# Optimization experiments

Hardware: AMD Instinct MI355X
Metric: run time of the kernel (lower is better)

## Reference

```python
import jax, jax.numpy as jnp
import numpy as np

TOPK_RATIOS = (0.67, 0.75, 0.8)


def setup_inputs() -> dict:
    key = jax.random.key(0)
    k0, k1, k2 = jax.random.split(key, 3)
    B, L, S, H, E, D = 4, 2048, 2048, 8, 64, 64
    queries = jax.random.normal(k0, (B, L, H, E), dtype=jnp.float32)
    keys = jax.random.normal(k1, (B, S, H, E), dtype=jnp.float32)
    values = jax.random.normal(k2, (B, S, H, D), dtype=jnp.float32)
    attn_weights = jnp.ones((len(TOPK_RATIOS),), dtype=jnp.float32)  # nn.Parameter(ones)
    attn_mask = jnp.zeros((1,), dtype=bool)  # unused by the module
    return {"queries": queries, "keys": keys, "values": values,
            "attn_weights": attn_weights, "attn_mask": attn_mask}


def reference(queries, keys, values, attn_weights, attn_mask):
    # queries: [B,L,H,E], keys: [B,S,H,E], values: [B,S,H,D]
    B, L, H, E = queries.shape
    S = keys.shape[1]
    scale = 1.0 / np.sqrt(E)  # self.scale is None -> 1/sqrt(E)
    scores = jnp.einsum('blhe,bshe->bhls', queries, keys) * scale  # [B,H,L,S]
    out = jnp.zeros(queries.shape[:3] + (values.shape[-1],), dtype=scores.dtype)
    for i, ratio in enumerate(TOPK_RATIOS):
        k = int(S * ratio)
        topv = jax.lax.top_k(scores, k)[0]            # sorted descending
        kth = topv[..., -1:]                           # k-th largest per row
        # mask==0 -> -inf, then softmax over S (ties at threshold are measure-zero)
        masked = jnp.where(scores >= kth, scores, -jnp.inf)
        attn = jax.nn.softmax(masked, axis=-1)         # dropout = identity (eval)
        out = out + jnp.einsum('bhls,bshd->blhd', attn, values) * attn_weights[i]
    return out
```

## Files before the change

kernel.cpp:

```cpp
#include <hip/hip_runtime.h>
#include <hip/hip_fp16.h>

typedef _Float16 f16x8 __attribute__((ext_vector_type(8)));
typedef float f32x4 __attribute__((ext_vector_type(4)));

#define KSEL0 1372u
#define KSEL1 1536u
#define KSEL2 1638u
#define WSC 16.0f
#define CSH 8.0f

__device__ __forceinline__ unsigned ou16_of(unsigned hb) {
  return hb ^ ((hb & 0x8000u) ? 0xFFFFu : 0x8000u);
}
__device__ __forceinline__ unsigned ou16_inv(unsigned ou) {
  return (ou & 0x8000u) ? (ou ^ 0x8000u) : (ou ^ 0xFFFFu);
}
__device__ __forceinline__ unsigned pk2(float a, float b) {
  auto h = __builtin_amdgcn_cvt_pkrtz(a, b);
  return __builtin_bit_cast(unsigned, h);
}
__device__ __forceinline__ unsigned shflx(unsigned v, int m) {
  return (unsigned)__shfl_xor((int)v, m, 64);
}

__device__ __forceinline__ unsigned sel_digit_s(const unsigned* histw, unsigned k,
                                                int lane, int shift) {
  uint4 hr = ((const uint4*)histw)[lane];
  unsigned hx = (hr.x >> shift) & 0xFFFFu;
  unsigned hy = (hr.y >> shift) & 0xFFFFu;
  unsigned hz = (hr.z >> shift) & 0xFFFFu;
  unsigned hw_ = (hr.w >> shift) & 0xFFFFu;
  unsigned s4 = hx + hy + hz + hw_;
  unsigned p = s4;
  #pragma unroll
  for (int off = 1; off < 64; off <<= 1) {
    int sl = lane + off;
    unsigned t = (unsigned)__shfl((int)p, sl < 64 ? sl : lane, 64);
    p += (sl < 64) ? t : 0u;
  }
  unsigned a3 = p - s4;
  unsigned a2 = a3 + hw_;
  unsigned a1 = a2 + hz;
  unsigned a0 = a1 + hy;
  int d = -1; unsigned nk = 0;
  if (a3 < k && a3 + hw_ >= k)      { d = 4*lane+3; nk = k - a3; }
  else if (a2 < k && a2 + hz >= k)  { d = 4*lane+2; nk = k - a2; }
  else if (a1 < k && a1 + hy >= k)  { d = 4*lane+1; nk = k - a1; }
  else if (a0 < k && a0 + hx >= k)  { d = 4*lane+0; nk = k - a0; }
  unsigned long long mb = __ballot(d >= 0);
  int src = __ffsll(mb) - 1;
  unsigned pack = ((unsigned)d << 16) | nk;
  return (unsigned)__shfl((int)pack, src, 64);
}

extern "C" __global__ __launch_bounds__(256)
void prep_k(const float* __restrict__ K, unsigned short* __restrict__ Kh) {
  int idx = blockIdx.x * 256 + threadIdx.x;
  int ec = idx & 7;
  int s  = (idx >> 3) & 2047;
  int bh = idx >> 14;
  int b = bh >> 3, h = bh & 7;
  const float* src = K + (((size_t)b * 2048 + s) * 8 + h) * 64 + ec * 8;
  float4 a = *(const float4*)src;
  float4 c = *(const float4*)(src + 4);
  uint4 val = { pk2(a.x, a.y), pk2(a.z, a.w), pk2(c.x, c.y), pk2(c.z, c.w) };
  *(uint4*)(Kh + (size_t)idx * 8) = val;
}

extern "C" __global__ __launch_bounds__(256)
void prep_v(const float* __restrict__ V, unsigned short* __restrict__ Vt) {
  const int tid  = threadIdx.x;
  const int w    = tid >> 6;
  const int lane = tid & 63;
  const int u_   = lane >> 4;
  const int dq   = (lane >> 2) & 3;
  const int r_   = lane & 3;
  const unsigned selv = (lane & 1) ? 0x03020706u : 0x05040100u;

  int bh = blockIdx.x >> 4;
  int s0 = (blockIdx.x & 15) * 128;
  int b = bh >> 3, h = bh & 7;
  const float* Vb = V + ((size_t)b * 2048 * 8 + h) * 64;
  unsigned short* Vo = Vt + (size_t)bh * 64 * 2048;

  #pragma unroll
  for (int sp = 0; sp < 2; ++sp) {
    #pragma unroll
    for (int p = 0; p < 4; ++p) {
      int sl = w * 32 + sp * 16 + u_ * 4;
      int sg = s0 + sl + r_;
      int d0 = p * 16 + dq * 4;
      float4 f = *(const float4*)(Vb + (size_t)sg * 512 + d0);
      unsigned lo = pk2(f.x, f.y), hi = pk2(f.z, f.w);
      unsigned tlo = shflx(lo, 1), thi = shflx(hi, 1);
      lo = __builtin_amdgcn_perm(tlo, lo, selv);
      hi = __builtin_amdgcn_perm(thi, hi, selv);
      unsigned t2lo = shflx(lo, 2), t2hi = shflx(hi, 2);
      unsigned Aw = (lane & 2) ? t2hi : lo;
      unsigned Bw = (lane & 2) ? hi   : t2lo;
      int d = d0 + r_;
      uint2 wv = {Aw, Bw};
      *(uint2*)(Vo + (size_t)d * 2048 + s0 + sl) = wv;
    }
  }
}

extern "C" __global__ __launch_bounds__(512, 4)
void nma_kernel(const float* __restrict__ Q, const unsigned short* __restrict__ Kh,
                const unsigned short* __restrict__ Vt, const float* __restrict__ AW,
                float* __restrict__ Out)
{
  __shared__ __align__(16) char lds[81920];
  unsigned* work = (unsigned*)(lds + 65536);

  const int tid  = threadIdx.x;
  const int w    = tid >> 6;
  const int lane = tid & 63;
  const int g    = lane >> 4;
  const int lx   = lane & 15;

  int bid = blockIdx.x;
  int lb  = (bid & 7) * 512 + (bid >> 3);
  int bh  = lb >> 7;
  int b   = bh >> 3, hh = bh & 7;
  int l0  = (lb & 127) << 4;

  const float* Qb = Q + (((size_t)b * 2048 + l0) * 8 + hh) * 64;
  const unsigned short* Khb = Kh + (size_t)bh * 2048 * 64;
  const unsigned short* Vtb = Vt + (size_t)bh * 64 * 2048;

  {
    uint4 z4 = {0u,0u,0u,0u};
    uint4* p = (uint4*)work;
    p[tid] = z4;
    p[tid + 512] = z4;
  }

  union FU { f16x8 v; unsigned u[4]; };
  FU qa0, qa1;
  {
    const float* qp = Qb + (size_t)lx * 512 + g * 8;
    float4 a = *(const float4*)(qp);
    float4 c = *(const float4*)(qp + 4);
    qa0.u[0] = pk2(a.x*0.125f, a.y*0.125f); qa0.u[1] = pk2(a.z*0.125f, a.w*0.125f);
    qa0.u[2] = pk2(c.x*0.125f, c.y*0.125f); qa0.u[3] = pk2(c.z*0.125f, c.w*0.125f);
    a = *(const float4*)(qp + 32);
    c = *(const float4*)(qp + 36);
    qa1.u[0] = pk2(a.x*0.125f, a.y*0.125f); qa1.u[1] = pk2(a.z*0.125f, a.w*0.125f);
    qa1.u[2] = pk2(c.x*0.125f, c.y*0.125f); qa1.u[3] = pk2(c.z*0.125f, c.w*0.125f);
  }
  __syncthreads();

  const unsigned swl = (((unsigned)(lx & 7)) << 4) | (((unsigned)(lx & 8)) << 3);
  unsigned* hq = work + lx * 256;
  #pragma unroll 2
  for (int t = 0; t < 16; ++t) {
    int s0 = (t * 8 + w) * 16;
    const unsigned short* kp = Khb + (size_t)(s0 + lx) * 64 + g * 8;
    f16x8 kb0 = *(const f16x8*)(kp);
    f16x8 kb1 = *(const f16x8*)(kp + 32);
    f32x4 acc = {0.f, 0.f, 0.f, 0.f};
    acc = __builtin_amdgcn_mfma_f32_16x16x32_f16(kb0, qa0.v, acc, 0, 0, 0);
    acc = __builtin_amdgcn_mfma_f32_16x16x32_f16(kb1, qa1.v, acc, 0, 0, 0);
    unsigned u0 = pk2(acc[0], acc[1]);
    unsigned u1 = pk2(acc[2], acc[3]);
    uint2 wv = {u0, u1};
    *(uint2*)(lds + lx * 4096 + (((unsigned)(s0 * 2 + g * 8)) ^ swl)) = wv;
    atomicAdd(&hq[ou16_of(u0 & 0xFFFFu) >> 8], 1u);
    atomicAdd(&hq[ou16_of(u0 >> 16) >> 8], 1u);
    atomicAdd(&hq[ou16_of(u1 & 0xFFFFu) >> 8], 1u);
    atomicAdd(&hq[ou16_of(u1 >> 16) >> 8], 1u);
  }
  __syncthreads();

  const float aw0 = AW[0], aw1 = AW[1], aw2 = AW[2];

  unsigned d0a[2], d1a[2], d2a[2], k0a[2], k1a[2], k2a[2];
  #pragma unroll 2
  for (int rr = 0; rr < 2; ++rr) {
    int q = 2 * w + rr;
    const unsigned* hw1 = work + q * 256;
    unsigned p0 = sel_digit_s(hw1, KSEL0, lane, 0);
    unsigned p1 = sel_digit_s(hw1, KSEL1, lane, 0);
    unsigned p2 = sel_digit_s(hw1, KSEL2, lane, 0);
    d0a[rr] = p0 >> 16; k0a[rr] = p0 & 0xFFFFu;
    d1a[rr] = p1 >> 16; k1a[rr] = p1 & 0xFFFFu;
    d2a[rr] = p2 >> 16; k2a[rr] = p2 & 0xFFFFu;
  }

  unsigned* hw2 = work + w * 512;
  #pragma unroll 1
  for (int rr = 0; rr < 2; ++rr) {
    int q = 2 * w + rr;
    const unsigned swq = (((unsigned)(q & 7)) << 4) | (((unsigned)(q & 8)) << 3);
    char* rowp = lds + q * 4096;
    for (int i = lane; i < 512; i += 64) hw2[i] = 0u;
    unsigned D0 = d0a[rr], D1 = d1a[rr], D2 = d2a[rr];
    for (int it = 0; it < 4; ++it) {
      uint4 dv = *(const uint4*)(rowp + (((unsigned)(it * 1024 + lane * 16)) ^ swq));
      unsigned ws[4] = {dv.x, dv.y, dv.z, dv.w};
      #pragma unroll
      for (int p = 0; p < 4; ++p) {
        #pragma unroll
        for (int hp = 0; hp < 2; ++hp) {
          unsigned bits = (ws[p] >> (hp * 16)) & 0xFFFFu;
          unsigned ou = ou16_of(bits);
          unsigned hi = ou >> 8, lo = ou & 255u;
          unsigned add = (hi == D0 ? 1u : 0u) | (hi == D1 ? 0x10000u : 0u);
          if (add) atomicAdd(&hw2[lo], add);
          if (hi == D2) atomicAdd(&hw2[256 + lo], 1u);
        }
      }
    }
    unsigned T1o = (D0 << 8) | (sel_digit_s(hw2,       k0a[rr], lane, 0)  >> 16);
    unsigned T2o = (D1 << 8) | (sel_digit_s(hw2,       k1a[rr], lane, 16) >> 16);
    unsigned T3o = (D2 << 8) | (sel_digit_s(hw2 + 256, k2a[rr], lane, 0)  >> 16);
    float zbA = 0.f, zbB = 0.f, zbC = 0.f;
    for (int it = 0; it < 4; ++it) {
      char* ap = rowp + (((unsigned)(it * 1024 + lane * 16)) ^ swq);
      uint4 dv = *(const uint4*)ap;
      unsigned ws[4] = {dv.x, dv.y, dv.z, dv.w};
      uint4 nv;
      unsigned no[4];
      #pragma unroll
      for (int p = 0; p < 4; ++p) {
        unsigned b0 = ws[p] & 0xFFFFu, b1 = ws[p] >> 16;
        float s0 = __half2float(__ushort_as_half((unsigned short)b0));
        float s1 = __half2float(__ushort_as_half((unsigned short)b1));
        float e0 = __expf(s0 - CSH), e1 = __expf(s1 - CSH);
        unsigned o0 = ou16_of(b0), o1 = ou16_of(b1);
        if (o0 >= T1o) zbA += e0; else if (o0 >= T2o) zbB += e0; else if (o0 >= T3o) zbC += e0;
        if (o1 >= T1o) zbA += e1; else if (o1 >= T2o) zbB += e1; else if (o1 >= T3o) zbC += e1;
        no[p] = pk2(e0, e1);
      }
      nv.x = no[0]; nv.y = no[1]; nv.z = no[2]; nv.w = no[3];
      *(uint4*)ap = nv;
    }
    #pragma unroll
    for (int off = 1; off < 64; off <<= 1) {
      zbA += __shfl_xor(zbA, off, 64);
      zbB += __shfl_xor(zbB, off, 64);
      zbC += __shfl_xor(zbC, off, 64);
    }
    float z1 = zbA, z2 = zbA + zbB, z3 = z2 + zbC;
    float A3 = aw2 / z3;
    float A2 = aw1 / z2 + A3;
    float A1 = aw0 / z1 + A2;
    A1 *= WSC; A2 *= WSC; A3 *= WSC;
    float T1f = __half2float(__ushort_as_half((unsigned short)ou16_inv(T1o)));
    float T2f = __half2float(__ushort_as_half((unsigned short)ou16_inv(T2o)));
    float T3f = __half2float(__ushort_as_half((unsigned short)ou16_inv(T3o)));
    unsigned e1b = pk2(__expf(T1f - CSH), 0.f) & 0xFFFFu;
    unsigned e2b = pk2(__expf(T2f - CSH), 0.f) & 0xFFFFu;
    unsigned e3b = pk2(__expf(T3f - CSH), 0.f) & 0xFFFFu;
    for (int it = 0; it < 4; ++it) {
      char* ap = rowp + (((unsigned)(it * 1024 + lane * 16)) ^ swq);
      uint4 dv = *(const uint4*)ap;
      unsigned ws[4] = {dv.x, dv.y, dv.z, dv.w};
      uint4 nv;
      unsigned no[4];
      #pragma unroll
      for (int p = 0; p < 4; ++p) {
        unsigned b0 = ws[p] & 0xFFFFu, b1 = ws[p] >> 16;
        float e0 = __half2float(__ushort_as_half((unsigned short)b0));
        float e1 = __half2float(__ushort_as_half((unsigned short)b1));
        float c0 = (b0 >= e1b) ? A1 : (b0 >= e2b) ? A2 : (b0 >= e3b) ? A3 : 0.f;
        float c1 = (b1 >= e1b) ? A1 : (b1 >= e2b) ? A2 : (b1 >= e3b) ? A3 : 0.f;
        no[p] = pk2(e0 * c0, e1 * c1);
      }
      nv.x = no[0]; nv.y = no[1]; nv.z = no[2]; nv.w = no[3];
      *(uint4*)ap = nv;
    }
  }
  __syncthreads();

  f32x4 oacc = {0.f, 0.f, 0.f, 0.f};
  const int dt = (w >> 1) * 16;
  const int sh = w & 1;
  const unsigned short* vp = Vtb + (size_t)(dt + lx) * 2048 + sh * 1024 + g * 8;
  const char* bp = lds + lx * 4096;

  #pragma unroll 8
  for (int kc = 0; kc < 32; ++kc) {
    f16x8 av = *(const f16x8*)(vp + kc * 32);
    unsigned sb = (unsigned)((sh * 1024 + kc * 32 + g * 8) * 2);
    f16x8 bv = *(const f16x8*)(bp + (sb ^ swl));
    oacc = __builtin_amdgcn_mfma_f32_16x16x32_f16(av, bv, oacc, 0, 0, 0);
  }

  float* pbuf = (float*)work;
  *(f32x4*)(pbuf + w * 256 + lx * 16 + g * 4) = oacc;
  __syncthreads();
  if (w < 4) {
    const float* pa = pbuf + (2 * w) * 256 + lx * 16 + g * 4;
    float4 ra = *(const float4*)pa;
    float4 rb = *(const float4*)(pa + 256);
    float* op = Out + (((size_t)b * 2048 + l0 + lx) * 8 + hh) * 64 + w * 16 + g * 4;
    float4 ov = { (ra.x + rb.x) * (1.f/WSC), (ra.y + rb.y) * (1.f/WSC),
                  (ra.z + rb.z) * (1.f/WSC), (ra.w + rb.w) * (1.f/WSC) };
    *(float4*)op = ov;
  }
}

extern "C" void kernel_launch(void* const* d_in, const int* in_sizes, int n_in,
                              void* d_out, int out_size, void* d_ws, size_t ws_size,
                              hipStream_t stream) {
  (void)in_sizes; (void)n_in; (void)out_size; (void)ws_size;
  const float* Q  = (const float*)d_in[0];
  const float* K  = (const float*)d_in[1];
  const float* V  = (const float*)d_in[2];
  const float* AW = (const float*)d_in[3];
  unsigned short* Kh = (unsigned short*)d_ws;
  unsigned short* Vt = (unsigned short*)((char*)d_ws + 8388608);
  prep_k<<<dim3(2048), dim3(256), 0, stream>>>(K, Kh);
  prep_v<<<dim3(512),  dim3(256), 0, stream>>>(V, Vt);
  nma_kernel<<<dim3(4096), dim3(512), 0, stream>>>(Q, Kh, Vt, AW, (float*)d_out);
}
```

Before: 390.6 us.

## Fuse exp into histogram pass and keep row values in registers

Computes exp of scores during the second-level histogram pass and keeps the packed fp16 results in 16 registers. This removes one LDS read/write sweep per row, and the partition sums now compare exp values directly against exp thresholds. The final scaling uses a packed half2 multiply with fp16 coefficients instead of float math. The LDS swizzle is also reduced to only the lx&7 term, which may change bank conflict behaviour. The costs are extra register pressure and slightly different rounding, since the coefficients are now held in fp16.

```diff
diff --git a/kernel.cpp b/kernel.cpp
--- a/kernel.cpp
+++ b/kernel.cpp
@@ -22,6 +22,9 @@
 }
 __device__ __forceinline__ unsigned shflx(unsigned v, int m) {
   return (unsigned)__shfl_xor((int)v, m, 64);
+}
+__device__ __forceinline__ float h2f(unsigned bits16) {
+  return __half2float(__ushort_as_half((unsigned short)bits16));
 }
 
 __device__ __forceinline__ unsigned sel_digit_s(const unsigned* histw, unsigned k,
@@ -152,7 +155,7 @@
   }
   __syncthreads();
 
-  const unsigned swl = (((unsigned)(lx & 7)) << 4) | (((unsigned)(lx & 8)) << 3);
+  const unsigned swl = ((unsigned)(lx & 7)) << 4;
   unsigned* hq = work + lx * 256;
   #pragma unroll 2
   for (int t = 0; t < 16; ++t) {
@@ -193,49 +196,48 @@
   #pragma unroll 1
   for (int rr = 0; rr < 2; ++rr) {
     int q = 2 * w + rr;
-    const unsigned swq = (((unsigned)(q & 7)) << 4) | (((unsigned)(q & 8)) << 3);
+    const unsigned swq = ((unsigned)(q & 7)) << 4;
     char* rowp = lds + q * 4096;
     for (int i = lane; i < 512; i += 64) hw2[i] = 0u;
     unsigned D0 = d0a[rr], D1 = d1a[rr], D2 = d2a[rr];
+
+    unsigned ereg[16];
+    #pragma unroll
     for (int it = 0; it < 4; ++it) {
       uint4 dv = *(const uint4*)(rowp + (((unsigned)(it * 1024 + lane * 16)) ^ swq));
       unsigned ws[4] = {dv.x, dv.y, dv.z, dv.w};
       #pragma unroll
       for (int p = 0; p < 4; ++p) {
-        #pragma unroll
-        for (int hp = 0; hp < 2; ++hp) {
-          unsigned bits = (ws[p] >> (hp * 16)) & 0xFFFFu;
-          unsigned ou = ou16_of(bits);
-          unsigned hi = ou >> 8, lo = ou & 255u;
-          unsigned add = (hi == D0 ? 1u : 0u) | (hi == D1 ? 0x10000u : 0u);
-          if (add) atomicAdd(&hw2[lo], add);
-          if (hi == D2) atomicAdd(&hw2[256 + lo], 1u);
-        }
+        unsigned b0 = ws[p] & 0xFFFFu, b1 = ws[p] >> 16;
+        unsigned o0 = ou16_of(b0), o1 = ou16_of(b1);
+        unsigned hi0 = o0 >> 8, lo0 = o0 & 255u;
+        unsigned hi1 = o1 >> 8, lo1 = o1 & 255u;
+        unsigned add0 = (hi0 == D0 ? 1u : 0u) | (hi0 == D1 ? 0x10000u : 0u);
+        unsigned add1 = (hi1 == D0 ? 1u : 0u) | (hi1 == D1 ? 0x10000u : 0u);
+        if (add0) atomicAdd(&hw2[lo0], add0);
+        if (hi0 == D2) atomicAdd(&hw2[256 + lo0], 1u);
+        if (add1) atomicAdd(&hw2[lo1], add1);
+        if (hi1 == D2) atomicAdd(&hw2[256 + lo1], 1u);
+        float e0 = __expf(h2f(b0) - CSH);
+        float e1 = __expf(h2f(b1) - CSH);
+        ereg[it * 4 + p] = pk2(e0, e1);
       }
     }
     unsigned T1o = (D0 << 8) | (sel_digit_s(hw2,       k0a[rr], lane, 0)  >> 16);
     unsigned T2o = (D1 << 8) | (sel_digit_s(hw2,       k1a[rr], lane, 16) >> 16);
     unsigned T3o = (D2 << 8) | (sel_digit_s(hw2 + 256, k2a[rr], lane, 0)  >> 16);
+    unsigned e1b = pk2(__expf(h2f(ou16_inv(T1o)) - CSH), 0.f) & 0xFFFFu;
+    unsigned e2b = pk2(__expf(h2f(ou16_inv(T2o)) - CSH), 0.f) & 0xFFFFu;
+    unsigned e3b = pk2(__expf(h2f(ou16_inv(T3o)) - CSH), 0.f) & 0xFFFFu;
+
     float zbA = 0.f, zbB = 0.f, zbC = 0.f;
-    for (int it = 0; it < 4; ++it) {
-      char* ap = rowp + (((unsigned)(it * 1024 + lane * 16)) ^ swq);
-      uint4 dv = *(const uint4*)ap;
-      unsigned ws[4] = {dv.x, dv.y, dv.z, dv.w};
-      uint4 nv;
-      unsigned no[4];
-      #pragma unroll
-      for (int p = 0; p < 4; ++p) {
-        unsigned b0 = ws[p] & 0xFFFFu, b1 = ws[p] >> 16;
-        float s0 = __half2float(__ushort_as_half((unsigned short)b0));
-        float s1 = __half2float(__ushort_as_half((unsigned short)b1));
-        float e0 = __expf(s0 - CSH), e1 = __expf(s1 - CSH);
-        unsigned o0 = ou16_of(b0), o1 = ou16_of(b1);
-        if (o0 >= T1o) zbA += e0; else if (o0 >= T2o) zbB += e0; else if (o0 >= T3o) zbC += e0;
-        if (o1 >= T1o) zbA += e1; else if (o1 >= T2o) zbB += e1; else if (o1 >= T3o) zbC += e1;
-        no[p] = pk2(e0, e1);
-      }
-      nv.x = no[0]; nv.y = no[1]; nv.z = no[2]; nv.w = no[3];
-      *(uint4*)ap = nv;
+    #pragma unroll
+    for (int i = 0; i < 16; ++i) {
+      unsigned uu = ereg[i];
+      unsigned b0 = uu & 0xFFFFu, b1 = uu >> 16;
+      float e0 = h2f(b0), e1 = h2f(b1);
+      if (b0 >= e1b) zbA += e0; else if (b0 >= e2b) zbB += e0; else if (b0 >= e3b) zbC += e0;
+      if (b1 >= e1b) zbA += e1; else if (b1 >= e2b) zbB += e1; else if (b1 >= e3b) zbC += e1;
     }
     #pragma unroll
     for (int off = 1; off < 64; off <<= 1) {
@@ -247,30 +249,25 @@
     float A3 = aw2 / z3;
     float A2 = aw1 / z2 + A3;
     float A1 = aw0 / z1 + A2;
-    A1 *= WSC; A2 *= WSC; A3 *= WSC;
-    float T1f = __half2float(__ushort_as_half((unsigned short)ou16_inv(T1o)));
-    float T2f = __half2float(__ushort_as_half((unsigned short)ou16_inv(T2o)));
-    float T3f = __half2float(__ushort_as_half((unsigned short)ou16_inv(T3o)));
-    unsigned e1b = pk2(__expf(T1f - CSH), 0.f) & 0xFFFFu;
-    unsigned e2b = pk2(__expf(T2f - CSH), 0.f) & 0xFFFFu;
-    unsigned e3b = pk2(__expf(T3f - CSH), 0.f) & 0xFFFFu;
+    unsigned A1b = pk2(A1 * WSC, 0.f) & 0xFFFFu;
+    unsigned A2b = pk2(A2 * WSC, 0.f) & 0xFFFFu;
+    unsigned A3b = pk2(A3 * WSC, 0.f) & 0xFFFFu;
+
+    #pragma unroll
     for (int it = 0; it < 4; ++it) {
-      char* ap = rowp + (((unsigned)(it * 1024 + lane * 16)) ^ swq);
-      uint4 dv = *(const uint4*)ap;
-      unsigned ws[4] = {dv.x, dv.y, dv.z, dv.w};
-      uint4 nv;
       unsigned no[4];
       #pragma unroll
       for (int p = 0; p < 4; ++p) {
-        unsigned b0 = ws[p] & 0xFFFFu, b1 = ws[p] >> 16;
-        float e0 = __half2float(__ushort_as_half((unsigned short)b0));
-        float e1 = __half2float(__ushort_as_half((unsigned short)b1));
-        float c0 = (b0 >= e1b) ? A1 : (b0 >= e2b) ? A2 : (b0 >= e3b) ? A3 : 0.f;
-        float c1 = (b1 >= e1b) ? A1 : (b1 >= e2b) ? A2 : (b1 >= e3b) ? A3 : 0.f;
-        no[p] = pk2(e0 * c0, e1 * c1);
+        unsigned uu = ereg[it * 4 + p];
+        unsigned b0 = uu & 0xFFFFu, b1 = uu >> 16;
+        unsigned c0 = (b0 >= e1b) ? A1b : (b0 >= e2b) ? A2b : (b0 >= e3b) ? A3b : 0u;
+        unsigned c1 = (b1 >= e1b) ? A1b : (b1 >= e2b) ? A2b : (b1 >= e3b) ? A3b : 0u;
+        unsigned cw = c0 | (c1 << 16);
+        __half2 prod = *(__half2*)&uu * *(__half2*)&cw;
+        no[p] = *(unsigned*)&prod;
       }
-      nv.x = no[0]; nv.y = no[1]; nv.z = no[2]; nv.w = no[3];
-      *(uint4*)ap = nv;
+      uint4 nv = {no[0], no[1], no[2], no[3]};
+      *(uint4*)(rowp + (((unsigned)(it * 1024 + lane * 16)) ^ swq)) = nv;
     }
   }
   __syncthreads();
```

Result: faster. 375.0 us (-4.0%).
